# Kernel tuning notes

Measured on AMD Instinct MI355X. Metric: run time of the kernel, lower is better.

Reference implementation:

```python
import jax, jax.numpy as jnp
import numpy as np

EPS = 1e-5
BIG = np.int32(2 ** 30)      # sentinel larger than any voxel label
L_MAX = 1024                  # fixed upper bound on number of components (jit-friendly)


def _offsets(conn):
    # 3D neighborhood offsets with at most `conn` nonzero coordinates (skimage connectivity)
    offs = []
    for dz in (-1, 0, 1):
        for dy in (-1, 0, 1):
            for dx in (-1, 0, 1):
                nz = (dz != 0) + (dy != 0) + (dx != 0)
                if 0 < nz <= conn:
                    offs.append((dz, dy, dx))
    return offs


def _ccl_26(fg):
    """Connected-component labeling, 26-connectivity (skimage.label connectivity=3).
    Iterative min-label propagation (3x3x3 min-pool) + pointer jumping.
    Returns int32 labels: 0 = background, each component gets min(flat_index)+1."""
    shape = fg.shape
    n = fg.size
    init = jnp.where(fg, jnp.arange(1, n + 1, dtype=jnp.int32).reshape(shape), 0)

    def step(labels):
        cand = jnp.where(fg, labels, BIG)
        pooled = jax.lax.reduce_window(cand, BIG, jax.lax.min, (3, 3, 3), (1, 1, 1), 'SAME')
        new = jnp.where(fg, jnp.minimum(labels, pooled), 0)
        flat = new.ravel()
        for _ in range(2):  # pointer jumping / path compression (labels are flat_index+1)
            parent = flat[jnp.maximum(flat - 1, 0)]
            flat = jnp.where(flat > 0, parent, 0)
        return flat.reshape(shape)

    def cond(c):
        old, new = c
        return jnp.any(old != new)

    def body(c):
        _, cur = c
        return cur, step(cur)

    _, final = jax.lax.while_loop(cond, body, (init, step(init)))
    return final


def _inner_boundary_18(fg):
    """skimage find_boundaries(mode='inner', connectivity=2) on 3D binary mask:
    foreground voxel with any background voxel in its 18-neighborhood
    (fg & ~erosion(fg), reflect border handling)."""
    D, H, W = fg.shape
    p = jnp.pad(fg, 1, mode='reflect')
    eroded = fg
    for dz, dy, dx in _offsets(2):
        eroded = eroded & p[1 + dz:1 + dz + D, 1 + dy:1 + dy + H, 1 + dx:1 + dx + W]
    return fg & ~eroded


def _compactness(y_pred):
    fg = y_pred > 0.5
    labels = _ccl_26(fg)                       # [D,H,W] int32
    boundary = _inner_boundary_18(fg)          # [D,H,W] bool

    # compact per-component ids (sorted unique labels, padded with BIG to stay sorted)
    uniq = jnp.unique(labels, size=L_MAX, fill_value=BIG)
    ids = jnp.searchsorted(uniq, labels).astype(jnp.int32)

    area = jax.ops.segment_sum(fg.astype(jnp.float32).ravel(), ids.ravel(), num_segments=L_MAX)
    perim = jax.ops.segment_sum(boundary.astype(jnp.float32).ravel(), ids.ravel(), num_segments=L_MAX)

    valid = (uniq > 0) & (uniq < BIG)
    # sum over z of 4*pi*area_z / (perim_3d^2 + eps) == 4*pi*total_area / (perim^2 + eps),
    # then averaged over depth D (as in the original per-label /= shape[0]).
    per_label = jnp.where(valid, 4.0 * jnp.pi * area / (perim ** 2 + EPS), 0.0)
    return jnp.sum(per_label) / y_pred.shape[0]


def setup_inputs() -> dict:
    key = jax.random.key(0)
    y_pred = jax.random.uniform(key, (64, 256, 256), dtype=jnp.float32)
    return {"y_pred": y_pred}


def reference(y_pred) -> jnp.ndarray:
    comp = _compactness(y_pred)
    return 1.0 / (comp + EPS)
```

## Files before the change

### kernel.cpp

```cpp
#include <hip/hip_runtime.h>

#define DD 64
#define HH 256
#define WW 256
#define NN (DD*HH*WW)
#define GHS 4096
#define NCOPY 16
#define PHS 131072
#define NSEG (NN/32)

#define TZ 8
#define TY 32
#define TX 32
#define TVOX (TZ*TY*TX)

#define CA 458752
#define CB 114688
#define CFACE (CA + 4*CB)

__device__ __forceinline__ int ufind(int* P, int x){
  int p = P[x];
  while (p != x){
    int gp = P[p];
    if (gp != p) P[x] = gp;
    x = gp;
    p = P[x];
  }
  return x;
}

__device__ __forceinline__ int ufind_ro(const int* P, int x){
  int p = P[x];
  while (p != x){ x = p; p = P[x]; }
  return x;
}

__device__ __forceinline__ void uunion(int* P, int a, int b){
  while (true){
    a = ufind(P, a);
    b = ufind(P, b);
    if (a == b) return;
    if (a < b){ int t = a; a = b; b = t; }
    int old = atomicMin(&P[a], b);
    if (old == a) return;
    a = old;
  }
}

__device__ __forceinline__ int run_start(unsigned m, int x){
  unsigned zb = (~m) & ((x == 0) ? 0u : ((1u << x) - 1u));
  return (zb == 0) ? 0 : (32 - __builtin_clz(zb));
}

__device__ __forceinline__ int refl(int v, int L){ return v < 0 ? 1 : (v >= L ? L - 2 : v); }

__global__ __launch_bounds__(1024) void k_local(const float* __restrict__ in,
                                                int* __restrict__ parent,
                                                unsigned* __restrict__ fgbits,
                                                int* __restrict__ hkey,
                                                int* __restrict__ harea,
                                                int* __restrict__ hper,
                                                unsigned long long* __restrict__ ph){
  __shared__ int sl[TVOX];
  __shared__ unsigned srow[256];
  __shared__ int q[4096];
  __shared__ int qn;
  const int t = threadIdx.x;
  const int lane = t & 63;
  const int b = blockIdx.x;
  const int z0 = (b >> 6) * TZ;
  const int y0 = ((b >> 3) & 7) * TY;
  const int x0 = (b & 7) * TX;

  if (b < (NCOPY * GHS) / 1024){ int j = b * 1024 + t; hkey[j] = -1; harea[j] = 0; hper[j] = 0; }
  { int j = b * 1024 + t; if (j < PHS) ph[j] = ~0ULL; }
  if (t == 0) qn = 0;

  const int row = t >> 2;
  const int xb  = (t & 3) * 8;
  const int lz  = row >> 5, ly = row & 31;
  const int gi0 = ((z0 + lz) << 16) | ((y0 + ly) << 8) | (x0 + xb);

  float4 f0 = *(const float4*)(in + gi0);
  float4 f1 = *(const float4*)(in + gi0 + 4);
  int by = (f0.x > 0.5f)        | ((f0.y > 0.5f) << 1) |
           ((f0.z > 0.5f) << 2) | ((f0.w > 0.5f) << 3) |
           ((f1.x > 0.5f) << 4) | ((f1.y > 0.5f) << 5) |
           ((f1.z > 0.5f) << 6) | ((f1.w > 0.5f) << 7);
  int v1 = by | (__shfl_xor(by, 1) << 8);
  int v2 = v1 | (__shfl_xor(v1, 2) << 16);
  if ((t & 3) == 0){
    srow[row] = (unsigned)v2;
    fgbits[((z0 + lz) << 11) | ((y0 + ly) << 3) | (x0 >> 5)] = (unsigned)v2;
  }
  __syncthreads();

  const unsigned m = srow[row];
  const unsigned starts = m & ~(m << 1);
  const unsigned sm = starts & (0xFFu << xb);

  {
    int cnt = __popc(sm);
    int pre = cnt;
    #pragma unroll
    for (int d = 1; d < 64; d <<= 1){
      int v = __shfl_up(pre, d);
      if (lane >= d) pre += v;
    }
    int tot = __shfl(pre, 63);
    int bw = 0;
    if (lane == 63) bw = atomicAdd(&qn, tot);
    bw = __shfl(bw, 63);
    int pos = bw + pre - cnt;
    unsigned w = sm;
    while (w){
      int s = __builtin_ctz(w); w &= w - 1;
      int v = (row << 5) | s;
      sl[v] = v;
      q[pos++] = v;
    }
  }
  __syncthreads();
  const int NQ = qn;

  const int rel[4][2] = {{-1,-1},{-1,0},{-1,1},{0,-1}};
  for (int it = t; it < NQ; it += 1024){
    int v = q[it];
    int vrow = v >> 5, x = v & 31;
    unsigned mr = srow[vrow];
    unsigned zs = (~mr) >> x;
    int len = zs ? __builtin_ctz(zs) : (32 - x);
    int end = x + len - 1;
    unsigned long long wmask = ((1ull << (end + 2)) - 1) &
                               ~((x == 0) ? 0ull : ((1ull << (x - 1)) - 1));
    int vlz = vrow >> 5, vly = vrow & 31;
    #pragma unroll
    for (int r = 0; r < 4; r++){
      int zz = vlz + rel[r][0], yy = vly + rel[r][1];
      if (zz < 0 || yy < 0 || yy >= TY) continue;
      int nrow = (zz << 5) | yy;
      unsigned mN = srow[nrow];
      unsigned wm = mN & (unsigned)wmask;
      while (wm){
        int bb = __builtin_ctz(wm);
        int ns = run_start(mN, bb);
        uunion(sl, v, (nrow << 5) | ns);
        unsigned t2 = (~mN) >> bb;
        int l2 = t2 ? __builtin_ctz(t2) : (32 - bb);
        unsigned long long clr = (bb + l2 >= 32) ? 0xffffffffull : ((1ull << (bb + l2)) - 1);
        wm &= ~(unsigned)clr;
      }
    }
  }
  __syncthreads();

  for (int it = t; it < NQ; it += 1024){
    int v = q[it];
    sl[v] = ufind_ro(sl, v);
  }
  __syncthreads();

  int lab[8];
  int cur = -1;
  #pragma unroll
  for (int k = 0; k < 8; k++){
    int x = xb + k;
    if (!((m >> x) & 1)){ lab[k] = -1; cur = -1; continue; }
    if (cur < 0){
      int rs = (k == 0) ? run_start(m, x) : x;
      int r = sl[(row << 5) | rs];
      cur = ((z0 + (r >> 10)) << 16) | ((y0 + ((r >> 5) & 31)) << 8) | (x0 + (r & 31));
    }
    lab[k] = cur;
  }
  *(int4*)(parent + gi0)     = make_int4(lab[0], lab[1], lab[2], lab[3]);
  *(int4*)(parent + gi0 + 4) = make_int4(lab[4], lab[5], lab[6], lab[7]);
}

__device__ __forceinline__ void phash_union(unsigned long long* H, unsigned long long key,
                                            int* parent){
  unsigned h = (unsigned)((key * 0x9E3779B97F4A7C15ull) >> 47);
  while (true){
    unsigned long long old = atomicCAS(&H[h], ~0ULL, key);
    if (old == ~0ULL){ uunion(parent, (int)(key >> 32), (int)(key & 0xffffffffu)); return; }
    if (old == key) return;
    h = (h + 1) & (PHS - 1);
  }
}

__global__ __launch_bounds__(256) void k_pairs(int* __restrict__ parent,
                                               const unsigned* __restrict__ fgbits,
                                               unsigned long long* __restrict__ ph){
  __shared__ unsigned long long pk[256];
  const int t = threadIdx.x;
  pk[t] = ~0ULL;
  __syncthreads();

  const int id = blockIdx.x * 256 + t;
  int z, y, x, ot;
  if (id < CA){ ot = 0; z = ((id >> 16) + 1) << 3; y = (id >> 8) & 255; x = id & 255; }
  else {
    int q = id - CA;
    int f = q >> 14;
    int r = q & 16383;
    int g = f / 7, mm = f % 7;
    if      (g == 0){ ot = 1; y = (mm + 1) << 5;  z = r >> 8; x = r & 255; }
    else if (g == 1){ ot = 2; y = (mm << 5) + 31; z = r >> 8; x = r & 255; }
    else if (g == 2){ ot = 3; x = (mm + 1) << 5;  z = r >> 8; y = r & 255; }
    else            { ot = 4; x = (mm << 5) + 31; z = r >> 8; y = r & 255; }
  }
  const int s = x >> 5, xl = x & 31;
  const unsigned wself = fgbits[(z << 11) | (y << 3) | s];
  if ((wself >> xl) & 1){
    const int a = parent[(z << 16) | (y << 8) | x];
    unsigned long long lastkey = ~0ULL;

    auto do_pair = [&](int zz, int yy, int xc){
      int bl = parent[(zz << 16) | (yy << 8) | xc];
      int hi = a > bl ? a : bl, lo = a > bl ? bl : a;
      unsigned long long key = ((unsigned long long)(unsigned)hi << 32) | (unsigned)lo;
      if (key == lastkey) return;
      lastkey = key;
      unsigned h = (unsigned)((key * 0x9E3779B97F4A7C15ull) >> 56);
      for (int probe = 0; probe < 256; probe++){
        unsigned long long old = atomicCAS(&pk[h], ~0ULL, key);
        if (old == ~0ULL || old == key) return;
        h = (h + 1) & 255;
      }
      phash_union(ph, key, parent);
    };

    auto do_row = [&](int zz, int yy){
      if (zz < 0 || yy < 0 || yy >= HH) return;
      unsigned mN = fgbits[(zz << 11) | (yy << 3) | s];
      if ((mN >> xl) & 1){ do_pair(zz, yy, x); return; }
      bool l = (xl > 0) ? ((mN >> (xl - 1)) & 1)
                        : (x > 0 && ((fgbits[(zz << 11) | (yy << 3) | (s - 1)] >> 31) & 1));
      bool r = (xl < 31) ? ((mN >> (xl + 1)) & 1)
                         : (x < WW - 1 && (fgbits[(zz << 11) | (yy << 3) | (s + 1)] & 1));
      if (l) do_pair(zz, yy, x - 1);
      if (r) do_pair(zz, yy, x + 1);
    };

    auto do_bit = [&](int zz, int yy, int xc){
      if (zz < 0 || yy < 0 || yy >= HH) return;
      unsigned mN = fgbits[(zz << 11) | (yy << 3) | (xc >> 5)];
      if ((mN >> (xc & 31)) & 1) do_pair(zz, yy, xc);
    };

    switch (ot){
      case 0: do_row(z-1, y-1); do_row(z-1, y); do_row(z-1, y+1); break;
      case 1: do_row(z-1, y-1); do_row(z, y-1); break;
      case 2: do_row(z-1, y+1); break;
      case 3: do_bit(z-1, y-1, x-1); do_bit(z-1, y, x-1); do_bit(z-1, y+1, x-1);
              do_bit(z,   y-1, x-1); do_bit(z,   y, x-1); break;
      case 4: do_bit(z-1, y-1, x+1); do_bit(z-1, y, x+1); do_bit(z-1, y+1, x+1);
              do_bit(z,   y-1, x+1); break;
    }
  }
  __syncthreads();
  if (pk[t] != ~0ULL) phash_union(ph, pk[t], parent);
}

__device__ __forceinline__ void ghash_add(int* hkey, int* harea, int* hper,
                                          int key, int a, int p){
  unsigned h = ((unsigned)key * 2654435761u) >> 20;
  while (true){
    int old = atomicCAS(&hkey[h], -1, key);
    if (old == -1 || old == key){
      atomicAdd(&harea[h], a);
      if (p) atomicAdd(&hper[h], p);
      return;
    }
    h = (h + 1) & (GHS - 1);
  }
}

__global__ __launch_bounds__(1024) void k_stats(const int* __restrict__ parent,
                                                const unsigned* __restrict__ fgbits,
                                                int* __restrict__ hkey,
                                                int* __restrict__ harea,
                                                int* __restrict__ hper){
  __shared__ unsigned sfg[144];
  __shared__ unsigned sbnd[32];
  __shared__ int sk[256], sa[256], sp[256];
  const int t = threadIdx.x;
  const int b = blockIdx.x;
  const int z = b >> 6;
  const int y0 = (b & 63) * 4;

  if (t < 256){ sk[t] = -1; sa[t] = 0; sp[t] = 0; }
  if (t < 144){
    int p = t / 48, q = (t / 8) % 6, s = t & 7;
    int zz = refl(z + p - 1, DD), yy = refl(y0 + q - 1, HH);
    sfg[t] = fgbits[(zz << 11) | (yy << 3) | s];
  }
  __syncthreads();

  if (t < 32){
    int ry = t >> 3, s = t & 7;
    auto W  = [&](int p, int q){ return sfg[p * 48 + q * 8 + s]; };
    auto WL = [&](int p, int q){
      unsigned w = W(p, q);
      unsigned c = (s > 0) ? ((sfg[p * 48 + q * 8 + s - 1] >> 31) & 1u) : ((w >> 1) & 1u);
      return (w << 1) | c;
    };
    auto WR = [&](int p, int q){
      unsigned w = W(p, q);
      unsigned c = (s < 7) ? ((sfg[p * 48 + q * 8 + s + 1] & 1u) << 31) : ((w & 0x40000000u) << 1);
      return (w >> 1) | c;
    };
    int qm = ry, qc = ry + 1, qp = ry + 2;
    unsigned own = W(1, qc);
    unsigned e = W(0, qm) & W(0, qp) & W(2, qm) & W(2, qp);
    e &= W(0, qc) & WL(0, qc) & WR(0, qc);
    e &= W(2, qc) & WL(2, qc) & WR(2, qc);
    e &= W(1, qm) & WL(1, qm) & WR(1, qm);
    e &= W(1, qp) & WL(1, qp) & WR(1, qp);
    e &= WL(1, qc) & WR(1, qc);
    sbnd[t] = own & ~e;
  }
  __syncthreads();

  const int i = b * 1024 + t;
  int lab = parent[i];
  int bnd = 0;
  if (lab >= 0){
    bnd = (sbnd[t >> 5] >> (t & 31)) & 1;
    int p = parent[lab];
    while (p != lab){ lab = p; p = parent[lab]; }
  }

  const int lane = t & 63;
  unsigned long long fgm = __ballot(lab >= 0);
  unsigned long long bm  = __ballot(bnd != 0);
  unsigned long long act = fgm;
  while (act){
    int leader = (int)__ffsll(act) - 1;
    int llab = __shfl(lab, leader);
    unsigned long long match = __ballot(lab == llab) & fgm;
    if (lane == leader){
      int a = (int)__popcll(match);
      int p = (int)__popcll(match & bm);
      unsigned h = ((unsigned)llab * 2654435761u) >> 24;
      bool done = false;
      for (int probe = 0; probe < 256; probe++){
        int old = atomicCAS(&sk[h], -1, llab);
        if (old == -1 || old == llab){
          atomicAdd(&sa[h], a);
          if (p) atomicAdd(&sp[h], p);
          done = true; break;
        }
        h = (h + 1) & 255;
      }
      if (!done) ghash_add(hkey, harea, hper, llab, a, p);
    }
    act &= ~match;
  }
  __syncthreads();
  const int c = (b & (NCOPY - 1)) * GHS;
  if (t < 256 && sk[t] >= 0) ghash_add(hkey + c, harea + c, hper + c, sk[t], sa[t], sp[t]);
}

__global__ __launch_bounds__(256) void k_merge(int* __restrict__ hkey,
                                               int* __restrict__ harea,
                                               int* __restrict__ hper){
  const int j = GHS + blockIdx.x * 256 + threadIdx.x;
  int key = hkey[j];
  if (key >= 0) ghash_add(hkey, harea, hper, key, harea[j], hper[j]);
}

__global__ __launch_bounds__(256) void k_fin(const int* __restrict__ hkey,
                                             const int* __restrict__ harea,
                                             const int* __restrict__ hper,
                                             float* __restrict__ out){
  __shared__ float ssum[256];
  const int t = threadIdx.x;
  float s = 0.0f;
  for (int j = t; j < GHS; j += 256){
    if (hkey[j] >= 0){
      float a = (float)harea[j];
      float p = (float)hper[j];
      s += 12.566370614359172f * a / (p * p + 1e-5f);
    }
  }
  ssum[t] = s;
  __syncthreads();
  for (int w = 128; w > 0; w >>= 1){
    if (t < w) ssum[t] += ssum[t + w];
    __syncthreads();
  }
  if (t == 0){
    float comp = ssum[0] / 64.0f;
    out[0] = 1.0f / (comp + 1e-5f);
  }
}

extern "C" void kernel_launch(void* const* d_in, const int* in_sizes, int n_in,
                              void* d_out, int out_size, void* d_ws, size_t ws_size,
                              hipStream_t stream){
  const float* y = (const float*)d_in[0];
  char* w = (char*)d_ws;
  int* parent            = (int*)w;                    w += (size_t)NN * 4;
  unsigned long long* ph = (unsigned long long*)w;     w += (size_t)PHS * 8;
  int* hkey              = (int*)w;                    w += (size_t)NCOPY * GHS * 4;
  int* harea             = (int*)w;                    w += (size_t)NCOPY * GHS * 4;
  int* hper              = (int*)w;                    w += (size_t)NCOPY * GHS * 4;
  unsigned* fgbits       = (unsigned*)w;               w += (size_t)NSEG * 4;
  float* out = (float*)d_out;

  hipLaunchKernelGGL(k_local, dim3(512),       dim3(1024), 0, stream, y, parent, fgbits, hkey, harea, hper, ph);
  hipLaunchKernelGGL(k_pairs, dim3(CFACE/256), dim3(256),  0, stream, parent, fgbits, ph);
  hipLaunchKernelGGL(k_stats, dim3(NN/1024),   dim3(1024), 0, stream, parent, fgbits, hkey, harea, hper);
  hipLaunchKernelGGL(k_merge, dim3((NCOPY-1)*GHS/256), dim3(256), 0, stream, hkey, harea, hper);
  hipLaunchKernelGGL(k_fin,   dim3(1),         dim3(256),  0, stream, hkey, harea, hper, out);
}
```

Before: 151.5 us.

## Fuse hash merge and final reduction into stats kernel via last-block pattern

Removes the separate merge and finalize kernels. The last block of the stats kernel, found with a global atomic counter, merges the sixteen hash copies in shared memory and computes the output. The global hash size is halved so the merge table fits in LDS, and the input floats are now read with nontemporal loads. This saves two kernel launches and the global atomic merge traffic. In exchange the merge runs serially in one block and the smaller table may see more probe collisions.

```diff
diff --git a/kernel.cpp b/kernel.cpp
--- a/kernel.cpp
+++ b/kernel.cpp
@@ -4,7 +4,7 @@
 #define HH 256
 #define WW 256
 #define NN (DD*HH*WW)
-#define GHS 4096
+#define GHS 2048
 #define NCOPY 16
 #define PHS 131072
 #define NSEG (NN/32)
@@ -17,6 +17,8 @@
 #define CA 458752
 #define CB 114688
 #define CFACE (CA + 4*CB)
+
+typedef float f4v __attribute__((ext_vector_type(4)));
 
 __device__ __forceinline__ int ufind(int* P, int x){
   int p = P[x];
@@ -60,7 +62,8 @@
                                                 int* __restrict__ hkey,
                                                 int* __restrict__ harea,
                                                 int* __restrict__ hper,
-                                                unsigned long long* __restrict__ ph){
+                                                unsigned long long* __restrict__ ph,
+                                                int* __restrict__ dcnt){
   __shared__ int sl[TVOX];
   __shared__ unsigned srow[256];
   __shared__ int q[4096];
@@ -74,6 +77,7 @@
 
   if (b < (NCOPY * GHS) / 1024){ int j = b * 1024 + t; hkey[j] = -1; harea[j] = 0; hper[j] = 0; }
   { int j = b * 1024 + t; if (j < PHS) ph[j] = ~0ULL; }
+  if (b == 0 && t == 0) dcnt[0] = 0;
   if (t == 0) qn = 0;
 
   const int row = t >> 2;
@@ -81,8 +85,9 @@
   const int lz  = row >> 5, ly = row & 31;
   const int gi0 = ((z0 + lz) << 16) | ((y0 + ly) << 8) | (x0 + xb);
 
-  float4 f0 = *(const float4*)(in + gi0);
-  float4 f1 = *(const float4*)(in + gi0 + 4);
+  const f4v* pv = (const f4v*)(in + gi0);
+  f4v f0 = __builtin_nontemporal_load(pv);
+  f4v f1 = __builtin_nontemporal_load(pv + 1);
   int by = (f0.x > 0.5f)        | ((f0.y > 0.5f) << 1) |
            ((f0.z > 0.5f) << 2) | ((f0.w > 0.5f) << 3) |
            ((f1.x > 0.5f) << 4) | ((f1.y > 0.5f) << 5) |
@@ -264,7 +269,7 @@
 
 __device__ __forceinline__ void ghash_add(int* hkey, int* harea, int* hper,
                                           int key, int a, int p){
-  unsigned h = ((unsigned)key * 2654435761u) >> 20;
+  unsigned h = ((unsigned)key * 2654435761u) >> 21;
   while (true){
     int old = atomicCAS(&hkey[h], -1, key);
     if (old == -1 || old == key){
@@ -280,7 +285,9 @@
                                                 const unsigned* __restrict__ fgbits,
                                                 int* __restrict__ hkey,
                                                 int* __restrict__ harea,
-                                                int* __restrict__ hper){
+                                                int* __restrict__ hper,
+                                                int* __restrict__ dcnt,
+                                                float* __restrict__ out){
   __shared__ unsigned sfg[144];
   __shared__ unsigned sbnd[32];
   __shared__ int sk[256], sa[256], sp[256];
@@ -360,39 +367,46 @@
   __syncthreads();
   const int c = (b & (NCOPY - 1)) * GHS;
   if (t < 256 && sk[t] >= 0) ghash_add(hkey + c, harea + c, hper + c, sk[t], sa[t], sp[t]);
-}
-
-__global__ __launch_bounds__(256) void k_merge(int* __restrict__ hkey,
-                                               int* __restrict__ harea,
-                                               int* __restrict__ hper){
-  const int j = GHS + blockIdx.x * 256 + threadIdx.x;
-  int key = hkey[j];
-  if (key >= 0) ghash_add(hkey, harea, hper, key, harea[j], hper[j]);
-}
-
-__global__ __launch_bounds__(256) void k_fin(const int* __restrict__ hkey,
-                                             const int* __restrict__ harea,
-                                             const int* __restrict__ hper,
-                                             float* __restrict__ out){
-  __shared__ float ssum[256];
-  const int t = threadIdx.x;
+
+  __shared__ int lastf;
+  __syncthreads();
+  if (t == 0) lastf = (atomicAdd(dcnt, 1) == (int)gridDim.x - 1);
+  __syncthreads();
+  if (!lastf) return;
+
+  __shared__ int mk[GHS], ma[GHS], mp[GHS];
+  for (int j = t; j < GHS; j += 1024){ mk[j] = -1; ma[j] = 0; mp[j] = 0; }
+  __syncthreads();
+  for (int j = t; j < NCOPY * GHS; j += 1024){
+    int key = __hip_atomic_load(&hkey[j], __ATOMIC_RELAXED, __HIP_MEMORY_SCOPE_AGENT);
+    if (key < 0) continue;
+    int a = __hip_atomic_load(&harea[j], __ATOMIC_RELAXED, __HIP_MEMORY_SCOPE_AGENT);
+    int p = __hip_atomic_load(&hper[j],  __ATOMIC_RELAXED, __HIP_MEMORY_SCOPE_AGENT);
+    unsigned h = ((unsigned)key * 2654435761u) >> 21;
+    while (true){
+      int old = atomicCAS(&mk[h], -1, key);
+      if (old == -1 || old == key){ atomicAdd(&ma[h], a); if (p) atomicAdd(&mp[h], p); break; }
+      h = (h + 1) & (GHS - 1);
+    }
+  }
+  __syncthreads();
   float s = 0.0f;
-  for (int j = t; j < GHS; j += 256){
-    if (hkey[j] >= 0){
-      float a = (float)harea[j];
-      float p = (float)hper[j];
+  for (int j = t; j < GHS; j += 1024){
+    if (mk[j] >= 0){
+      float a = (float)ma[j], p = (float)mp[j];
       s += 12.566370614359172f * a / (p * p + 1e-5f);
     }
   }
-  ssum[t] = s;
-  __syncthreads();
-  for (int w = 128; w > 0; w >>= 1){
-    if (t < w) ssum[t] += ssum[t + w];
-    __syncthreads();
-  }
+  #pragma unroll
+  for (int d2 = 32; d2 > 0; d2 >>= 1) s += __shfl_down(s, d2);
+  __shared__ float wsum[16];
+  if ((t & 63) == 0) wsum[t >> 6] = s;
+  __syncthreads();
   if (t == 0){
-    float comp = ssum[0] / 64.0f;
-    out[0] = 1.0f / (comp + 1e-5f);
+    float tot = 0.0f;
+    #pragma unroll
+    for (int k2 = 0; k2 < 16; k2++) tot += wsum[k2];
+    out[0] = 1.0f / (tot / 64.0f + 1e-5f);
   }
 }
 
@@ -407,11 +421,10 @@
   int* harea             = (int*)w;                    w += (size_t)NCOPY * GHS * 4;
   int* hper              = (int*)w;                    w += (size_t)NCOPY * GHS * 4;
   unsigned* fgbits       = (unsigned*)w;               w += (size_t)NSEG * 4;
+  int* dcnt              = (int*)w;                    w += 256;
   float* out = (float*)d_out;
 
-  hipLaunchKernelGGL(k_local, dim3(512),       dim3(1024), 0, stream, y, parent, fgbits, hkey, harea, hper, ph);
+  hipLaunchKernelGGL(k_local, dim3(512),       dim3(1024), 0, stream, y, parent, fgbits, hkey, harea, hper, ph, dcnt);
   hipLaunchKernelGGL(k_pairs, dim3(CFACE/256), dim3(256),  0, stream, parent, fgbits, ph);
-  hipLaunchKernelGGL(k_stats, dim3(NN/1024),   dim3(1024), 0, stream, parent, fgbits, hkey, harea, hper);
-  hipLaunchKernelGGL(k_merge, dim3((NCOPY-1)*GHS/256), dim3(256), 0, stream, hkey, harea, hper);
-  hipLaunchKernelGGL(k_fin,   dim3(1),         dim3(256),  0, stream, hkey, harea, hper, out);
-}
+  hipLaunchKernelGGL(k_stats, dim3(NN/1024),   dim3(1024), 0, stream, parent, fgbits, hkey, harea, hper, dcnt, out);
+}
```

After: 187.3 us. 23.6% more time.

## Defer root lookup to per-label flush, swizzle pair blocks, halve global hash

Applied to the files above, without the earlier changes.

k_stats no longer chases the union-find root for every voxel. It groups voxels by their provisional label in a shared hash and resolves the root only once per distinct label, when flushing to the global hash or on overflow. Overflow entries now also go into the block's copy of the hash rather than copy zero. k_pairs remaps block indices with an interleaved swizzle, and the global hash size is halved, which cuts merge and finalize work but raises the risk of collisions and of fill-up if many components exist.

```diff
diff --git a/kernel.cpp b/kernel.cpp
--- a/kernel.cpp
+++ b/kernel.cpp
@@ -4,7 +4,7 @@
 #define HH 256
 #define WW 256
 #define NN (DD*HH*WW)
-#define GHS 4096
+#define GHS 2048
 #define NCOPY 16
 #define PHS 131072
 #define NSEG (NN/32)
@@ -196,7 +196,9 @@
   pk[t] = ~0ULL;
   __syncthreads();
 
-  const int id = blockIdx.x * 256 + t;
+  const int nb = (int)gridDim.x;
+  const int bsw = (blockIdx.x & 7) * (nb >> 3) + (blockIdx.x >> 3);
+  const int id = bsw * 256 + t;
   int z, y, x, ot;
   if (id < CA){ ot = 0; z = ((id >> 16) + 1) << 3; y = (id >> 8) & 255; x = id & 255; }
   else {
@@ -264,7 +266,7 @@
 
 __device__ __forceinline__ void ghash_add(int* hkey, int* harea, int* hper,
                                           int key, int a, int p){
-  unsigned h = ((unsigned)key * 2654435761u) >> 20;
+  unsigned h = ((unsigned)key * 2654435761u) >> 21;
   while (true){
     int old = atomicCAS(&hkey[h], -1, key);
     if (old == -1 || old == key){
@@ -283,13 +285,14 @@
                                                 int* __restrict__ hper){
   __shared__ unsigned sfg[144];
   __shared__ unsigned sbnd[32];
-  __shared__ int sk[256], sa[256], sp[256];
+  __shared__ int dk[256], da[256], dp[256];
   const int t = threadIdx.x;
   const int b = blockIdx.x;
   const int z = b >> 6;
   const int y0 = (b & 63) * 4;
-
-  if (t < 256){ sk[t] = -1; sa[t] = 0; sp[t] = 0; }
+  const int c = (b & (NCOPY - 1)) * GHS;
+
+  if (t < 256){ dk[t] = -1; da[t] = 0; dp[t] = 0; }
   if (t < 144){
     int p = t / 48, q = (t / 8) % 6, s = t & 7;
     int zz = refl(z + p - 1, DD), yy = refl(y0 + q - 1, HH);
@@ -302,13 +305,13 @@
     auto W  = [&](int p, int q){ return sfg[p * 48 + q * 8 + s]; };
     auto WL = [&](int p, int q){
       unsigned w = W(p, q);
-      unsigned c = (s > 0) ? ((sfg[p * 48 + q * 8 + s - 1] >> 31) & 1u) : ((w >> 1) & 1u);
-      return (w << 1) | c;
+      unsigned c2 = (s > 0) ? ((sfg[p * 48 + q * 8 + s - 1] >> 31) & 1u) : ((w >> 1) & 1u);
+      return (w << 1) | c2;
     };
     auto WR = [&](int p, int q){
       unsigned w = W(p, q);
-      unsigned c = (s < 7) ? ((sfg[p * 48 + q * 8 + s + 1] & 1u) << 31) : ((w & 0x40000000u) << 1);
-      return (w >> 1) | c;
+      unsigned c2 = (s < 7) ? ((sfg[p * 48 + q * 8 + s + 1] & 1u) << 31) : ((w & 0x40000000u) << 1);
+      return (w >> 1) | c2;
     };
     int qm = ry, qc = ry + 1, qp = ry + 2;
     unsigned own = W(1, qc);
@@ -324,12 +327,7 @@
 
   const int i = b * 1024 + t;
   int lab = parent[i];
-  int bnd = 0;
-  if (lab >= 0){
-    bnd = (sbnd[t >> 5] >> (t & 31)) & 1;
-    int p = parent[lab];
-    while (p != lab){ lab = p; p = parent[lab]; }
-  }
+  int bnd = (lab >= 0) ? (int)((sbnd[t >> 5] >> (t & 31)) & 1) : 0;
 
   const int lane = t & 63;
   unsigned long long fgm = __ballot(lab >= 0);
@@ -345,21 +343,29 @@
       unsigned h = ((unsigned)llab * 2654435761u) >> 24;
       bool done = false;
       for (int probe = 0; probe < 256; probe++){
-        int old = atomicCAS(&sk[h], -1, llab);
+        int old = atomicCAS(&dk[h], -1, llab);
         if (old == -1 || old == llab){
-          atomicAdd(&sa[h], a);
-          if (p) atomicAdd(&sp[h], p);
+          atomicAdd(&da[h], a);
+          if (p) atomicAdd(&dp[h], p);
           done = true; break;
         }
         h = (h + 1) & 255;
       }
-      if (!done) ghash_add(hkey, harea, hper, llab, a, p);
+      if (!done){
+        int l2 = llab, pr = parent[l2];
+        while (pr != l2){ l2 = pr; pr = parent[l2]; }
+        ghash_add(hkey + c, harea + c, hper + c, l2, a, p);
+      }
     }
     act &= ~match;
   }
   __syncthreads();
-  const int c = (b & (NCOPY - 1)) * GHS;
-  if (t < 256 && sk[t] >= 0) ghash_add(hkey + c, harea + c, hper + c, sk[t], sa[t], sp[t]);
+  if (t < 256 && dk[t] >= 0){
+    int l2 = dk[t];
+    int pr = parent[l2];
+    while (pr != l2){ l2 = pr; pr = parent[l2]; }
+    ghash_add(hkey + c, harea + c, hper + c, l2, da[t], dp[t]);
+  }
 }
 
 __global__ __launch_bounds__(256) void k_merge(int* __restrict__ hkey,
```

New measurement: 158.1 us. +4.4%, slower.
